# Kernel tuning notes

Hardware: AMD Instinct MI355X
Metric: run time of the kernel (lower is better)

Reference implementation:

```python
import jax, jax.numpy as jnp
import numpy as np

B, C, H, W = 32, 512, 32, 32
S = 512  # number_of_spikes


def setup_inputs() -> dict:
    key = jax.random.key(0)
    k1, k2 = jax.random.split(key)
    # input must be non-negative (unnormalized probabilities over channel dim)
    x = jax.random.uniform(k1, (B, C, H, W), dtype=jnp.float32)
    # the torch module draws these internally with torch.rand; we pass them
    # explicitly so the reference is deterministic
    random_values = jax.random.uniform(k2, (B, S, H, W), dtype=jnp.float32)
    return {"x": x, "random_values": random_values}


def reference(x, random_values):
    # CDF over the channel dimension, normalized so the last entry is 1
    cdf = jnp.cumsum(x, axis=1)                     # [B, C, H, W]
    cdf = cdf / cdf[:, -1:, :, :]
    b, c, h, w = x.shape
    s = random_values.shape[1]
    # move channel/spike axis last and flatten pixels for vectorized searchsorted
    cdf_f = jnp.moveaxis(cdf, 1, -1).reshape(-1, c)             # [B*H*W, C]
    rv_f = jnp.moveaxis(random_values, 1, -1).reshape(-1, s)    # [B*H*W, S]
    # inverse-CDF sampling: first index i with cdf[i] >= u (binary search)
    idx = jax.vmap(lambda a, v: jnp.searchsorted(a, v, side="left"))(cdf_f, rv_f)
    spikes = jnp.moveaxis(idx.reshape(b, h, w, s), -1, 1)       # [B, S, H, W]
    return spikes.astype(jnp.int64)
```

## Files before the change

kernel.cpp:

```cpp
#include <hip/hip_runtime.h>

#define NB 32
#define NC 512
#define NS 512
#define HW 1024
#define P  16
#define BLOCK 256
#define ST 516
#define NBLK 2048

__device__ __forceinline__ int swz(int c) { return c ^ ((c >> 4) & 28); }

__global__ __launch_bounds__(BLOCK, 4) void spike_kernel(
    const float* __restrict__ x,
    const float* __restrict__ rv,
    int* __restrict__ out)
{
    __shared__ float cdf[P * ST];
    __shared__ float tot[P];

    const int tid = threadIdx.x;
    const int bid = blockIdx.x;
    const int logical = (bid & 7) * (NBLK / 8) + (bid >> 3);
    const int pix = logical * P;
    const int b  = pix >> 10;
    const int hw = pix & (HW - 1);
    const float* xb = x + (size_t)b * NC * HW + hw;

    {
        const int cq  = tid >> 2;
        const int px4 = (tid & 3) * 4;
        #pragma unroll
        for (int p = 0; p < 8; ++p) {
            const int c = p * 64 + cq;
            const float4 v = *(const float4*)(xb + (size_t)c * HW + px4);
            const int sc = swz(c);
            cdf[(px4 + 0) * ST + sc] = v.x;
            cdf[(px4 + 1) * ST + sc] = v.y;
            cdf[(px4 + 2) * ST + sc] = v.z;
            cdf[(px4 + 3) * ST + sc] = v.w;
        }
    }
    __syncthreads();

    if (tid < P) {
        float* row = cdf + tid * ST;
        float run = 0.f;
        #pragma unroll 4
        for (int c4 = 0; c4 < NC; c4 += 4) {
            float4 v = *(float4*)(row + swz(c4));
            float s0 = run + v.x;
            float s1 = s0 + v.y;
            float s2 = s1 + v.z;
            float s3 = s2 + v.w;
            run = s3;
            *(float4*)(row + swz(c4)) = make_float4(s0, s1, s2, s3);
        }
        tot[tid] = run;
    }
    __syncthreads();

    #pragma unroll
    for (int k = 0; k < 8; ++k) {
        const int flat = tid + k * BLOCK;
        const int px = flat >> 7;
        const int g  = flat & 127;
        const float t = tot[px];
        float4* ptr = (float4*)(cdf + px * ST + g * 4);
        float4 v = *ptr;
        v.x = v.x / t; v.y = v.y / t; v.z = v.z / t; v.w = v.w / t;
        *ptr = v;
    }
    __syncthreads();

    const int px  = tid & (P - 1);
    const int sof = tid >> 4;
    const float* row = cdf + px * ST;
    const float r255 = row[swz(255)];
    const float r127 = row[swz(127)], r383 = row[swz(383)];
    const float r63  = row[swz(63)],  r191 = row[swz(191)];
    const float r319 = row[swz(319)], r447 = row[swz(447)];
    const float r31  = row[swz(31)],  r95  = row[swz(95)];
    const float r159 = row[swz(159)], r223 = row[swz(223)];
    const float r287 = row[swz(287)], r351 = row[swz(351)];
    const float r415 = row[swz(415)], r479 = row[swz(479)];

    const size_t io_base = (size_t)b * NS * HW + hw + px;
    #pragma unroll 4
    for (int si = 0; si < 32; ++si) {
        const int s = si * 16 + sof;
        const size_t off = io_base + (size_t)s * HW;
        const float u = rv[off];
        const bool  b0 = r255 < u;
        const float p1 = b0 ? r383 : r127;
        const bool  b1 = p1 < u;
        const float p2a = b1 ? r191 : r63;
        const float p2b = b1 ? r447 : r319;
        const float p2  = b0 ? p2b : p2a;
        const bool  b2 = p2 < u;
        const float q0 = b2 ? r95  : r31;
        const float q1 = b2 ? r223 : r159;
        const float q2 = b2 ? r351 : r287;
        const float q3 = b2 ? r479 : r415;
        const float q01 = b1 ? q1 : q0;
        const float q23 = b1 ? q3 : q2;
        const float p3  = b0 ? q23 : q01;
        const bool  b3 = p3 < u;
        int pos = (b0 ? 256 : 0) | (b1 ? 128 : 0) | (b2 ? 64 : 0) | (b3 ? 32 : 0);
        #pragma unroll
        for (int step = 16; step > 0; step >>= 1) {
            const float a = row[swz(pos + step - 1)];
            pos += (a < u) ? step : 0;
        }
        out[off] = pos;
    }
}

extern "C" void kernel_launch(void* const* d_in, const int* in_sizes, int n_in,
                              void* d_out, int out_size, void* d_ws, size_t ws_size,
                              hipStream_t stream) {
    const float* x  = (const float*)d_in[0];
    const float* rv = (const float*)d_in[1];
    int* out = (int*)d_out;

    spike_kernel<<<dim3(NBLK), dim3(BLOCK), 0, stream>>>(x, rv, out);
}
```

Baseline: 196.6 us.

## Parallelize channel prefix scan across threads and skip CDF normalization

Each thread now loads 32 channels for one pixel into registers and computes a local sum. Segment offsets are combined with wave shuffles plus a small shared cross-wave table, replacing the serial 16-thread scan. The normalization pass is dropped by scaling the random value by the total instead of dividing every CDF entry. The shared CDF layout becomes channel-major with pixel as the fast index, which removes the swizzle. Comparing u*total against the unnormalized CDF can differ from the reference's normalized comparison at rounding boundaries.

```diff
diff --git a/kernel.cpp b/kernel.cpp
--- a/kernel.cpp
+++ b/kernel.cpp
@@ -6,91 +6,72 @@
 #define HW 1024
 #define P  16
 #define BLOCK 256
-#define ST 516
 #define NBLK 2048
-
-__device__ __forceinline__ int swz(int c) { return c ^ ((c >> 4) & 28); }
 
 __global__ __launch_bounds__(BLOCK, 4) void spike_kernel(
     const float* __restrict__ x,
     const float* __restrict__ rv,
     int* __restrict__ out)
 {
-    __shared__ float cdf[P * ST];
+    __shared__ float cdf[NC * P];
+    __shared__ float wtot[4 * P];
     __shared__ float tot[P];
 
-    const int tid = threadIdx.x;
+    const int tid  = threadIdx.x;
+    const int lane = tid & 63;
+    const int wv   = tid >> 6;
     const int bid = blockIdx.x;
     const int logical = (bid & 7) * (NBLK / 8) + (bid >> 3);
     const int pix = logical * P;
     const int b  = pix >> 10;
     const int hw = pix & (HW - 1);
-    const float* xb = x + (size_t)b * NC * HW + hw;
 
-    {
-        const int cq  = tid >> 2;
-        const int px4 = (tid & 3) * 4;
-        #pragma unroll
-        for (int p = 0; p < 8; ++p) {
-            const int c = p * 64 + cq;
-            const float4 v = *(const float4*)(xb + (size_t)c * HW + px4);
-            const int sc = swz(c);
-            cdf[(px4 + 0) * ST + sc] = v.x;
-            cdf[(px4 + 1) * ST + sc] = v.y;
-            cdf[(px4 + 2) * ST + sc] = v.z;
-            cdf[(px4 + 3) * ST + sc] = v.w;
-        }
-    }
+    const int px  = tid & 15;
+    const int seg = tid >> 4;
+
+    const float* xp = x + (size_t)b * NC * HW + (size_t)(seg * 32) * HW + hw + px;
+    float xs[32];
+    #pragma unroll
+    for (int i = 0; i < 32; ++i) xs[i] = xp[(size_t)i * HW];
+    float ssum = 0.f;
+    #pragma unroll
+    for (int i = 0; i < 32; ++i) ssum += xs[i];
+
+    float incl = ssum;
+    float t1 = __shfl_up(incl, 16, 64); incl += (lane >= 16) ? t1 : 0.f;
+    float t2 = __shfl_up(incl, 32, 64); incl += (lane >= 32) ? t2 : 0.f;
+    if (lane >= 48) wtot[wv * P + px] = incl;
     __syncthreads();
 
-    if (tid < P) {
-        float* row = cdf + tid * ST;
-        float run = 0.f;
-        #pragma unroll 4
-        for (int c4 = 0; c4 < NC; c4 += 4) {
-            float4 v = *(float4*)(row + swz(c4));
-            float s0 = run + v.x;
-            float s1 = s0 + v.y;
-            float s2 = s1 + v.z;
-            float s3 = s2 + v.w;
-            run = s3;
-            *(float4*)(row + swz(c4)) = make_float4(s0, s1, s2, s3);
-        }
-        tot[tid] = run;
-    }
+    float excl = incl - ssum;
+    for (int w = 0; w < wv; ++w) excl += wtot[w * P + px];
+
+    float run = excl;
+    float* cbase = cdf + seg * 32 * P + px;
+    #pragma unroll
+    for (int i = 0; i < 32; ++i) { run += xs[i]; cbase[i * P] = run; }
+    if (seg == 15) tot[px] = run;
     __syncthreads();
 
-    #pragma unroll
-    for (int k = 0; k < 8; ++k) {
-        const int flat = tid + k * BLOCK;
-        const int px = flat >> 7;
-        const int g  = flat & 127;
-        const float t = tot[px];
-        float4* ptr = (float4*)(cdf + px * ST + g * 4);
-        float4 v = *ptr;
-        v.x = v.x / t; v.y = v.y / t; v.z = v.z / t; v.w = v.w / t;
-        *ptr = v;
-    }
-    __syncthreads();
-
-    const int px  = tid & (P - 1);
-    const int sof = tid >> 4;
-    const float* row = cdf + px * ST;
-    const float r255 = row[swz(255)];
-    const float r127 = row[swz(127)], r383 = row[swz(383)];
-    const float r63  = row[swz(63)],  r191 = row[swz(191)];
-    const float r319 = row[swz(319)], r447 = row[swz(447)];
-    const float r31  = row[swz(31)],  r95  = row[swz(95)];
-    const float r159 = row[swz(159)], r223 = row[swz(223)];
-    const float r287 = row[swz(287)], r351 = row[swz(351)];
-    const float r415 = row[swz(415)], r479 = row[swz(479)];
+    const int sof = seg;
+    const float to = tot[px];
+    #define RC(p_) cdf[(p_) * P + px]
+    const float r255 = RC(255);
+    const float r127 = RC(127), r383 = RC(383);
+    const float r63  = RC(63),  r191 = RC(191);
+    const float r319 = RC(319), r447 = RC(447);
+    const float r31  = RC(31),  r95  = RC(95);
+    const float r159 = RC(159), r223 = RC(223);
+    const float r287 = RC(287), r351 = RC(351);
+    const float r415 = RC(415), r479 = RC(479);
+    #undef RC
 
     const size_t io_base = (size_t)b * NS * HW + hw + px;
     #pragma unroll 4
     for (int si = 0; si < 32; ++si) {
         const int s = si * 16 + sof;
         const size_t off = io_base + (size_t)s * HW;
-        const float u = rv[off];
+        const float u = rv[off] * to;
         const bool  b0 = r255 < u;
         const float p1 = b0 ? r383 : r127;
         const bool  b1 = p1 < u;
@@ -109,7 +90,7 @@
         int pos = (b0 ? 256 : 0) | (b1 ? 128 : 0) | (b2 ? 64 : 0) | (b3 ? 32 : 0);
         #pragma unroll
         for (int step = 16; step > 0; step >>= 1) {
-            const float a = row[swz(pos + step - 1)];
+            const float a = cdf[(pos + step - 1) * P + px];
             pos += (a < u) ? step : 0;
         }
         out[off] = pos;
```

Measured after the change: 188.9 us. 3.9% less time.
